# Kernel tuning notes

Measured on AMD Instinct MI355X. Metric: run time of the kernel, lower is better.

The kernel has to match this reference:

```python
import jax, jax.numpy as jnp
import numpy as np

STRIDE = 16
SCALES = (8, 16, 32)
RATIOS = (0.5, 1.0, 2.0)
PRE_NMS_TOPN = 6000
POST_NMS_TOPN = 300
NMS_THRESH = 0.7
MIN_SIZE = 16.0


def _mkanchors(ws, hs, xc, yc):
    ws = ws[:, None]; hs = hs[:, None]
    return np.hstack([xc - 0.5 * (ws - 1), yc - 0.5 * (hs - 1),
                      xc + 0.5 * (ws - 1), yc + 0.5 * (hs - 1)])


def _base_anchors():
    base = np.array([0.0, 0.0, STRIDE - 1.0, STRIDE - 1.0])
    w = base[2] - base[0] + 1; h = base[3] - base[1] + 1
    xc = base[0] + 0.5 * (w - 1); yc = base[1] + 0.5 * (h - 1)
    size = w * h
    ratios = np.array(RATIOS)
    ws = np.round(np.sqrt(size / ratios)); hs = np.round(ws * ratios)
    ra = _mkanchors(ws, hs, xc, yc)  # [3,4]
    out = []
    for a in ra:
        aw = a[2] - a[0] + 1; ah = a[3] - a[1] + 1
        axc = a[0] + 0.5 * (aw - 1); ayc = a[1] + 0.5 * (ah - 1)
        s = np.array(SCALES)
        out.append(_mkanchors(aw * s, ah * s, axc, ayc))
    return np.vstack(out).astype(np.float32)  # [9,4]


def _all_anchors(H, W):
    base = _base_anchors()  # [A,4]
    sx = np.arange(W) * STRIDE; sy = np.arange(H) * STRIDE
    gx, gy = np.meshgrid(sx, sy)  # [H,W]
    shifts = np.stack([gx.ravel(), gy.ravel(), gx.ravel(), gy.ravel()], axis=1)
    return (shifts[:, None, :].astype(np.float32) + base[None, :, :]).reshape(-1, 4)


def conv2d(x, w, b, pad):
    y = jax.lax.conv_general_dilated(x, w, (1, 1), [(pad, pad), (pad, pad)],
                                     dimension_numbers=('NCHW', 'OIHW', 'NCHW'))
    return y + b[None, :, None, None]


def rpn_forward(feature_map, im_info, conv_w, conv_b, cls_w, cls_b, bbox_w, bbox_b):
    x = jax.nn.relu(conv2d(feature_map, conv_w, conv_b, 1))
    cls_score = conv2d(x, cls_w, cls_b, 0)   # [1, 2A, H, W]
    bbox_pred = conv2d(x, bbox_w, bbox_b, 0)  # [1, 4A, H, W]
    b, c, H, W = cls_score.shape
    A = c // 2
    # softmax over (bg, fg) pairs: view(b,2,A,H,W), softmax dim=1
    prob = jax.nn.softmax(cls_score.reshape(b, 2, A, H, W), axis=1).reshape(b, c, H, W)
    scores = prob[0, A:].transpose(1, 2, 0).reshape(-1)       # fg scores [H*W*A]
    deltas = bbox_pred[0].transpose(1, 2, 0).reshape(-1, 4)   # [H*W*A, 4]
    anchors = jnp.asarray(_all_anchors(H, W))

    # bbox_transform_inv
    aw = anchors[:, 2] - anchors[:, 0] + 1.0
    ah = anchors[:, 3] - anchors[:, 1] + 1.0
    acx = anchors[:, 0] + 0.5 * aw
    acy = anchors[:, 1] + 0.5 * ah
    cx = deltas[:, 0] * aw + acx
    cy = deltas[:, 1] * ah + acy
    pw = jnp.exp(deltas[:, 2]) * aw
    ph = jnp.exp(deltas[:, 3]) * ah
    # clip to image
    x1 = jnp.clip(cx - 0.5 * pw, 0.0, im_info[1] - 1.0)
    y1 = jnp.clip(cy - 0.5 * ph, 0.0, im_info[0] - 1.0)
    x2 = jnp.clip(cx + 0.5 * pw, 0.0, im_info[1] - 1.0)
    y2 = jnp.clip(cy + 0.5 * ph, 0.0, im_info[0] - 1.0)
    boxes = jnp.stack([x1, y1, x2, y2], axis=1)

    # min-size filter (mask via -inf scores to keep shapes static)
    ms = MIN_SIZE * im_info[2]
    keep = ((x2 - x1 + 1.0) >= ms) & ((y2 - y1 + 1.0) >= ms)
    scores = jnp.where(keep, scores, -jnp.inf)

    # pre-NMS top-k (sorted descending)
    sc, idx = jax.lax.top_k(scores, PRE_NMS_TOPN)
    bx = boxes[idx]  # [P,4]
    areas = (bx[:, 2] - bx[:, 0] + 1.0) * (bx[:, 3] - bx[:, 1] + 1.0)

    def nms_step(supp, _):
        avail = jnp.where(supp, -jnp.inf, sc)
        i = jnp.argmax(avail)
        valid = avail[i] > -jnp.inf
        box = bx[i]
        xx1 = jnp.maximum(box[0], bx[:, 0]); yy1 = jnp.maximum(box[1], bx[:, 1])
        xx2 = jnp.minimum(box[2], bx[:, 2]); yy2 = jnp.minimum(box[3], bx[:, 3])
        inter = jnp.maximum(xx2 - xx1 + 1.0, 0.0) * jnp.maximum(yy2 - yy1 + 1.0, 0.0)
        iou = inter / (areas[i] + areas - inter)
        supp = supp | (iou > NMS_THRESH)  # suppresses i itself (iou==1)
        out_box = jnp.where(valid, box, jnp.zeros((4,), box.dtype))
        return supp, out_box

    supp0 = jnp.zeros((PRE_NMS_TOPN,), dtype=bool)
    _, kept = jax.lax.scan(nms_step, supp0, None, length=POST_NMS_TOPN)  # [300,4]
    rois = jnp.concatenate([jnp.zeros((POST_NMS_TOPN, 1), kept.dtype), kept], axis=1)
    return rois  # [300, 5] (batch_idx, x1, y1, x2, y2)


def setup_inputs() -> dict:
    key = jax.random.key(0)
    ks = jax.random.split(key, 7)
    C, A = 512, 9
    H, W = 64, 96  # feature map for a 1024x1536 image at stride 16
    std = 0.01  # weight_init gaussian std in the repo
    return {
        'feature_map': jax.random.normal(ks[0], (1, C, H, W), jnp.float32),
        'im_info': jnp.array([1024.0, 1536.0, 1.0], jnp.float32),
        'conv_w': std * jax.random.normal(ks[1], (C, C, 3, 3), jnp.float32),
        'conv_b': jnp.zeros((C,), jnp.float32),
        'cls_w': std * jax.random.normal(ks[2], (2 * A, C, 1, 1), jnp.float32),
        'cls_b': jnp.zeros((2 * A,), jnp.float32),
        'bbox_w': std * jax.random.normal(ks[3], (4 * A, C, 1, 1), jnp.float32),
        'bbox_b': jnp.zeros((4 * A,), jnp.float32),
    }


def reference(feature_map, im_info, conv_w, conv_b, cls_w, cls_b, bbox_w, bbox_b):
    return rpn_forward(feature_map, im_info, conv_w, conv_b, cls_w, cls_b, bbox_w, bbox_b)
```

## Files before the change

### kernel.cpp

```cpp
#include <hip/hip_runtime.h>
#include <stdint.h>

typedef unsigned int u32;
typedef unsigned long long u64;
typedef __attribute__((ext_vector_type(8))) short v8s;
typedef __attribute__((ext_vector_type(4))) float v4f;

#define HH 64
#define WW 96
#define HW 6144
#define CC 512
#define NANCH 55296
#define PRE 6000
#define POST 300
#define CAP 8192
#define PW 98
#define PH 66
#define ICPAD 40
#define NHB 384

__device__ __constant__ float c_aw[9] = {184.f,368.f,736.f,128.f,256.f,512.f,88.f,176.f,352.f};
__device__ __constant__ float c_ah[9] = {96.f,192.f,384.f,128.f,256.f,512.f,176.f,352.f,704.f};

__device__ __forceinline__ unsigned short bf16_rne(float x){
  u32 u = __float_as_uint(x);
  return (unsigned short)((u + 0x7FFFu + ((u >> 16) & 1u)) >> 16);
}
__device__ __forceinline__ u32 sortkey(float s){
  u32 u = __float_as_uint(s);
  return u ^ ((u & 0x80000000u) ? 0xFFFFFFFFu : 0x80000000u);
}

__global__ __launch_bounds__(256) void k_cvt(const float* __restrict__ X, const float* __restrict__ Wt,
                                             const float* __restrict__ cw, const float* __restrict__ bw,
                                             unsigned short* __restrict__ Xih, unsigned short* __restrict__ Xil,
                                             unsigned short* __restrict__ Wh2, unsigned short* __restrict__ Wl2,
                                             float* __restrict__ Whd, u32* __restrict__ zero_region){
  __shared__ float Ls[64][97];
  __shared__ float Ws[4608];
  const int b = blockIdx.x, tid = threadIdx.x;
  { int gid = b*256 + tid;
    if (gid < 163856) zero_region[gid] = 0u; }
  if (b < 528){
    const int rp  = b % 66;
    const int ic0 = (b / 66) * 64;
    const bool zrow = (rp == 0 || rp == PH-1);
    if (!zrow){
      int r = rp - 1;
      for (int i = tid; i < 6144; i += 256){
        int ii = i / 96, c = i - ii*96;
        Ls[ii][c] = X[(ic0+ii)*HW + r*WW + c];
      }
    }
    __syncthreads();
    for (int idx = tid; idx < 98*16; idx += 256){
      int cp = idx >> 4, g = idx & 15;
      int icl0 = g*4;
      u64 hv = 0, lv = 0;
      #pragma unroll
      for (int u = 0; u < 4; ++u){
        float x = 0.f;
        if (!zrow && cp >= 1 && cp <= 96) x = Ls[icl0+u][cp-1];
        unsigned short h = bf16_rne(x);
        float hf = __uint_as_float(((u32)h) << 16);
        unsigned short l = bf16_rne(x - hf);
        hv |= ((u64)h) << (16*u);
        lv |= ((u64)l) << (16*u);
      }
      long o = ((long)(rp*PW + cp) << 9) + ic0 + icl0;
      *reinterpret_cast<u64*>(Xih + o) = hv;
      *reinterpret_cast<u64*>(Xil + o) = lv;
    }
  } else if (b < 1040){
    const int oc = b - 528;
    for (int i = tid; i < 4608; i += 256) Ws[i] = Wt[oc*4608 + i];
    __syncthreads();
    for (int idx = tid; idx < 9*128; idx += 256){
      int tap = idx >> 7, g = idx & 127;
      int icb = g*4;
      u64 hv = 0, lv = 0;
      #pragma unroll
      for (int u = 0; u < 4; ++u){
        float x = Ws[(icb+u)*9 + tap];
        unsigned short h = bf16_rne(x);
        float hf = __uint_as_float(((u32)h) << 16);
        unsigned short l = bf16_rne(x - hf);
        hv |= ((u64)h) << (16*u);
        lv |= ((u64)l) << (16*u);
      }
      long o = ((long)(tap*512 + oc) << 9) + icb;
      *reinterpret_cast<u64*>(Wh2 + o) = hv;
      *reinterpret_cast<u64*>(Wl2 + o) = lv;
    }
  } else {
    int idx = (b - 1040)*256 + tid;
    int o  = idx >> 9;
    int gc = idx & 511;
    float v = 0.f;
    if (o < 18) v = cw[o*512 + gc];
    else if (o < 54) v = bw[(o-18)*512 + gc];
    Whd[gc*64 + o] = v;
  }
}

template<bool FIRST, bool LAST>
__global__ __launch_bounds__(256, 1) void k_conv3t(
    const unsigned short* __restrict__ Xih, const unsigned short* __restrict__ Xil,
    const unsigned short* __restrict__ Wh2, const unsigned short* __restrict__ Wl2,
    const float* __restrict__ Bc, float* __restrict__ Y)
{
  __shared__ __attribute__((aligned(16))) unsigned short Ah[6*98*ICPAD];
  __shared__ __attribute__((aligned(16))) unsigned short Al[6*98*ICPAD];
  __shared__ __attribute__((aligned(16))) unsigned short Bh[9*32*ICPAD];
  __shared__ __attribute__((aligned(16))) unsigned short Bl[9*32*ICPAD];
  const int tid  = threadIdx.x;
  const int w    = tid >> 6;
  const int lane = tid & 63;
  const int lm   = lane & 15;
  const int q    = lane >> 4;
  const int y0   = blockIdx.x * 4;
  const int oc0  = blockIdx.y * 32;
  const int yrow = y0 + w;

  v4f acc[6][2];
  if (FIRST){
    #pragma unroll
    for (int t = 0; t < 6; ++t)
      #pragma unroll
      for (int n = 0; n < 2; ++n)
        acc[t][n] = (v4f){0.f,0.f,0.f,0.f};
  } else {
    #pragma unroll
    for (int n = 0; n < 2; ++n){
      int oc = oc0 + n*16 + lm;
      #pragma unroll
      for (int t = 0; t < 6; ++t)
        acc[t][n] = *reinterpret_cast<const v4f*>(Y + (long)oc*HW + yrow*WW + 16*t + q*4);
    }
  }

  const int icg0 = FIRST ? 0 : 8;
  const int icgN = LAST ? 16 : 8;

  u64 ra[19][2], rb[9][2];
  auto loadSlab = [&](int icg){
    #pragma unroll
    for (int n = 0; n < 19; ++n){
      int it = tid + 256*n;
      if (it < 4704){
        int i4 = it & 7, rc = it >> 3;
        int c = rc % 98, r = rc / 98;
        long src = ((long)((y0 + r)*PW + c) << 9) + icg*32 + i4*4;
        ra[n][0] = *reinterpret_cast<const u64*>(Xih + src);
        ra[n][1] = *reinterpret_cast<const u64*>(Xil + src);
      }
    }
    #pragma unroll
    for (int n = 0; n < 9; ++n){
      int it = tid + 256*n;
      if (it < 2304){
        int i4 = it & 7, to = it >> 3;
        int oc = to & 31, tap = to >> 5;
        long src = ((long)(tap*512 + oc0 + oc) << 9) + icg*32 + i4*4;
        rb[n][0] = *reinterpret_cast<const u64*>(Wh2 + src);
        rb[n][1] = *reinterpret_cast<const u64*>(Wl2 + src);
      }
    }
  };
  auto storeSlab = [&](){
    #pragma unroll
    for (int n = 0; n < 19; ++n){
      int it = tid + 256*n;
      if (it < 4704){
        int i4 = it & 7, rc = it >> 3;
        int dst = rc*ICPAD + i4*4;
        *reinterpret_cast<u64*>(Ah + dst) = ra[n][0];
        *reinterpret_cast<u64*>(Al + dst) = ra[n][1];
      }
    }
    #pragma unroll
    for (int n = 0; n < 9; ++n){
      int it = tid + 256*n;
      if (it < 2304){
        int i4 = it & 7, to = it >> 3;
        int dst = to*ICPAD + i4*4;
        *reinterpret_cast<u64*>(Bh + dst) = rb[n][0];
        *reinterpret_cast<u64*>(Bl + dst) = rb[n][1];
      }
    }
  };

  loadSlab(icg0);
  for (int icg = icg0; icg < icgN; ++icg){
    __syncthreads();
    storeSlab();
    __syncthreads();
    if (icg + 1 < icgN) loadSlab(icg + 1);
    #pragma unroll
    for (int tap = 0; tap < 9; ++tap){
      const int dy = tap / 3, dx = tap - dy*3;
      v8s ah[6], al[6], bh[2], bl[2];
      #pragma unroll
      for (int t = 0; t < 6; ++t){
        int a = ((w + dy)*98 + 16*t + lm + dx)*ICPAD + q*8;
        ah[t] = *reinterpret_cast<const v8s*>(Ah + a);
        al[t] = *reinterpret_cast<const v8s*>(Al + a);
      }
      #pragma unroll
      for (int n = 0; n < 2; ++n){
        int a = (tap*32 + n*16 + lm)*ICPAD + q*8;
        bh[n] = *reinterpret_cast<const v8s*>(Bh + a);
        bl[n] = *reinterpret_cast<const v8s*>(Bl + a);
      }
      #pragma unroll
      for (int t = 0; t < 6; ++t)
        #pragma unroll
        for (int n = 0; n < 2; ++n){
          acc[t][n] = __builtin_amdgcn_mfma_f32_16x16x32_bf16(al[t], bl[n], acc[t][n], 0, 0, 0);
          acc[t][n] = __builtin_amdgcn_mfma_f32_16x16x32_bf16(al[t], bh[n], acc[t][n], 0, 0, 0);
          acc[t][n] = __builtin_amdgcn_mfma_f32_16x16x32_bf16(ah[t], bl[n], acc[t][n], 0, 0, 0);
          acc[t][n] = __builtin_amdgcn_mfma_f32_16x16x32_bf16(ah[t], bh[n], acc[t][n], 0, 0, 0);
        }
    }
  }

  #pragma unroll
  for (int n = 0; n < 2; ++n){
    int oc = oc0 + n*16 + lm;
    if (LAST){
      float b = Bc[oc];
      #pragma unroll
      for (int t = 0; t < 6; ++t){
        float4 v;
        v.x = fmaxf(acc[t][n].x + b, 0.f);
        v.y = fmaxf(acc[t][n].y + b, 0.f);
        v.z = fmaxf(acc[t][n].z + b, 0.f);
        v.w = fmaxf(acc[t][n].w + b, 0.f);
        *reinterpret_cast<float4*>(Y + (long)oc*HW + yrow*WW + 16*t + q*4) = v;
      }
    } else {
      #pragma unroll
      for (int t = 0; t < 6; ++t)
        *reinterpret_cast<v4f*>(Y + (long)oc*HW + yrow*WW + 16*t + q*4) = acc[t][n];
    }
  }
}

__global__ __launch_bounds__(256) void k_head(
    const float* __restrict__ Y, const float* __restrict__ Whd,
    const float* __restrict__ cb, const float* __restrict__ bb,
    const float* __restrict__ info,
    float* __restrict__ scores, float4* __restrict__ boxes, u32* __restrict__ hist8g)
{
  __shared__ float Ys[1024];
  __shared__ float Wsh[4096];
  __shared__ u32 lh[256];
  const int tid = threadIdx.x;
  const int p0  = blockIdx.x * 16;
  const int po  = tid & 15;
  const int oj  = tid >> 4;
  lh[tid] = 0u;
  float accM[4], accC[4];
  #pragma unroll
  for (int k = 0; k < 4; ++k){ accM[k] = 0.f; accC[k] = 0.f; }

  for (int c0 = 0; c0 < CC; c0 += 64){
    __syncthreads();
    for (int i = tid; i < 1024; i += 256){
      int c = i >> 4, p = i & 15;
      Ys[i] = Y[(c0 + c) * HW + p0 + p];
    }
    for (int i = tid; i < 4096; i += 256){
      int c = i >> 6, o = i & 63;
      Wsh[c*64 + (o & 15)*4 + (o >> 4)] = Whd[(c0 + c)*64 + o];
    }
    __syncthreads();
    #pragma unroll 4
    for (int c = 0; c < 64; ++c){
      float xa = Ys[c*16 + po];
      float4 wv = *reinterpret_cast<const float4*>(Wsh + c*64 + oj*4);
      accC[0] = __fmaf_rn(xa, wv.x, accC[0]);
      accC[1] = __fmaf_rn(xa, wv.y, accC[1]);
      accC[2] = __fmaf_rn(xa, wv.z, accC[2]);
      accC[3] = __fmaf_rn(xa, wv.w, accC[3]);
    }
    #pragma unroll
    for (int k = 0; k < 4; ++k){ accM[k] += accC[k]; accC[k] = 0.f; }
  }
  __syncthreads();
  #pragma unroll
  for (int k = 0; k < 4; ++k){
    int o = oj + 16*k;
    float bias = (o < 18) ? cb[o] : ((o < 54) ? bb[o - 18] : 0.f);
    Ys[po*64 + o] = accM[k] + bias;
  }
  __syncthreads();
  float imH = info[0], imW = info[1], imS = info[2];
  for (int it = tid; it < 144; it += 256){
    int pl = it / 9;
    int a  = it - pl*9;
    const float* L = Ys + pl*64;
    float l0 = L[a], l1 = L[9 + a];
    float mx = fmaxf(l0, l1);
    float e0 = expf(l0 - mx), e1 = expf(l1 - mx);
    float sc = e1 / (e0 + e1);
    float d0 = L[18 + a*4 + 0], d1 = L[18 + a*4 + 1];
    float d2 = L[18 + a*4 + 2], d3 = L[18 + a*4 + 3];
    int pos = p0 + pl;
    int yy = pos / 96;
    int xx = pos - yy * 96;
    float aw = c_aw[a], ah = c_ah[a];
    float acx = (float)(xx * 16 + 8);
    float acy = (float)(yy * 16 + 8);
    float cx = __fadd_rn(__fmul_rn(d0, aw), acx);
    float cy = __fadd_rn(__fmul_rn(d1, ah), acy);
    float pw = __fmul_rn(expf(d2), aw);
    float ph = __fmul_rn(expf(d3), ah);
    float hx = __fmul_rn(0.5f, pw);
    float hy = __fmul_rn(0.5f, ph);
    float x1 = fminf(fmaxf(__fadd_rn(cx, -hx), 0.f), imW - 1.f);
    float y1 = fminf(fmaxf(__fadd_rn(cy, -hy), 0.f), imH - 1.f);
    float x2 = fminf(fmaxf(__fadd_rn(cx,  hx), 0.f), imW - 1.f);
    float y2 = fminf(fmaxf(__fadd_rn(cy,  hy), 0.f), imH - 1.f);
    float ms = 16.f * imS;
    bool keep = ((x2 - x1 + 1.f) >= ms) && ((y2 - y1 + 1.f) >= ms);
    int g = pos * 9 + a;
    float val = keep ? sc : -__builtin_inff();
    scores[g] = val;
    boxes[g]  = make_float4(x1, y1, x2, y2);
    atomicAdd(&lh[sortkey(val) >> 24], 1u);
  }
  __syncthreads();
  hist8g[blockIdx.x*256 + tid] = lh[tid];
}

__global__ __launch_bounds__(1024) void k_sel(const u32* __restrict__ hist8g, u32* __restrict__ hist2,
                                              const float* __restrict__ scores,
                                              u32* __restrict__ ctr, u64* __restrict__ keys){
  __shared__ u32 cs[1024];
  __shared__ u32 bs[64];
  __shared__ u32 h8[256];
  __shared__ u32 lh2[256];
  __shared__ int selg;
  __shared__ u32 afterv, T16s, aboves, K32s, B8s, above8s;
  const int t = threadIdx.x;
  const int b0 = t * 64;

  { int g = t >> 8, bin = t & 255;
    u32 s = 0;
    for (int b = g; b < NHB; b += 4) s += hist8g[b*256 + bin];
    cs[t] = s; }
  __syncthreads();
  if (t < 256){
    h8[t] = cs[t] + cs[256 + t] + cs[512 + t] + cs[768 + t];
    lh2[t] = 0u;
  }
  __syncthreads();
  if (t == 0){
    u32 acc = 0;
    for (int bin = 255; bin >= 0; --bin){
      acc += h8[bin];
      if (acc >= 6000u){ B8s = (u32)bin; above8s = acc - h8[bin]; break; }
    }
  }
  __syncthreads();

  { u32 b8 = B8s;
    const float4* s4 = reinterpret_cast<const float4*>(scores);
    for (int i = t; i < NANCH/4; i += 1024){
      float4 v = s4[i];
      u32 k0 = sortkey(v.x), k1 = sortkey(v.y), k2 = sortkey(v.z), k3 = sortkey(v.w);
      if ((k0 >> 24) == b8) atomicAdd(&lh2[(k0 >> 16) & 0xFFu], 1u);
      if ((k1 >> 24) == b8) atomicAdd(&lh2[(k1 >> 16) & 0xFFu], 1u);
      if ((k2 >> 24) == b8) atomicAdd(&lh2[(k2 >> 16) & 0xFFu], 1u);
      if ((k3 >> 24) == b8) atomicAdd(&lh2[(k3 >> 16) & 0xFFu], 1u);
    } }
  __syncthreads();
  if (t == 0){
    u32 acc = above8s;
    for (int bin = 255; bin >= 0; --bin){
      acc += lh2[bin];
      if (acc >= 6000u){ T16s = (B8s << 8) | (u32)bin; aboves = acc - lh2[bin]; break; }
    }
  }
  __syncthreads();

  { u32 pfx = T16s;
    const float4* s4 = reinterpret_cast<const float4*>(scores);
    for (int i = t; i < NANCH/4; i += 1024){
      float4 v = s4[i];
      u32 k0 = sortkey(v.x), k1 = sortkey(v.y), k2 = sortkey(v.z), k3 = sortkey(v.w);
      if ((k0 >> 16) == pfx) atomicAdd(&hist2[k0 & 0xFFFFu], 1u);
      if ((k1 >> 16) == pfx) atomicAdd(&hist2[k1 & 0xFFFFu], 1u);
      if ((k2 >> 16) == pfx) atomicAdd(&hist2[k2 & 0xFFFFu], 1u);
      if ((k3 >> 16) == pfx) atomicAdd(&hist2[k3 & 0xFFFFu], 1u);
    } }
  __threadfence();
  __syncthreads();

  if (t == 0) selg = -1;
  __syncthreads();
  const u32 target = 6000u - aboves;
  { u32 s = 0;
    for (int i = 0; i < 64; ++i) s += hist2[b0 + i];
    cs[t] = s; }
  __syncthreads();
  for (int off = 1; off < 1024; off <<= 1){
    u32 v = cs[t];
    u32 ad = (t + off < 1024) ? cs[t + off] : 0u;
    __syncthreads();
    cs[t] = v + ad;
    __syncthreads();
  }
  { u32 here  = cs[t];
    u32 after = (t < 1023) ? cs[t + 1] : 0u;
    if (here >= target && after < target){ selg = t; afterv = after; } }
  __syncthreads();
  { int g = selg;
    if (g >= 0 && t < 64) bs[t] = hist2[g*64 + t];
    __syncthreads();
    if (t == 0){
      if (g < 0) K32s = (T16s << 16);
      else {
        u32 acc = afterv;
        for (int b = 63; b >= 0; --b){
          u32 h = bs[b];
          acc += h;
          if (acc >= target){ K32s = (T16s << 16) | (u32)(g*64 + b); break; }
        }
      }
      ctr[4] = 6000u;
    } }
  __syncthreads();

  { u32 K = K32s;
    const int lane = t & 63;
    const float4* s4 = reinterpret_cast<const float4*>(scores);
    for (int i = t; i < NANCH/4; i += 1024){
      float4 v = s4[i];
      u32 kk[4] = {sortkey(v.x), sortkey(v.y), sortkey(v.z), sortkey(v.w)};
      u64 m[4];
      #pragma unroll
      for (int u = 0; u < 4; ++u) m[u] = __ballot(kk[u] >= K);
      u32 tot = (u32)(__popcll(m[0]) + __popcll(m[1]) + __popcll(m[2]) + __popcll(m[3]));
      if (tot){
        u32 base = 0;
        if (lane == 0) base = atomicAdd(&ctr[0], tot);
        base = (u32)__shfl((int)base, 0, 64);
        u64 below = ((u64)1 << lane) - 1;
        u32 off = 0;
        #pragma unroll
        for (int u = 0; u < 4; ++u){
          if (kk[u] >= K){
            u32 pos = base + off + (u32)__popcll(m[u] & below);
            if (pos < CAP) keys[pos] = ((u64)kk[u] << 32) | (u64)(u32)(~(u32)(i*4 + u));
          }
          off += (u32)__popcll(m[u]);
        }
      }
    } }
}

__global__ __launch_bounds__(512) void k_rank(const u64* __restrict__ keys, u32* __restrict__ ctr,
                                              const float4* __restrict__ boxes,
                                              float4* __restrict__ topB, float* __restrict__ topA){
  __shared__ u64 ks[CAP];
  __shared__ u32 part[8][64];
  const int t  = threadIdx.x;
  const int s  = t >> 6;
  const int k  = t & 63;
  const int gi = blockIdx.x * 64 + k;
  u32 count = ctr[0]; if (count > CAP) count = CAP;
  u64 my = (gi < (int)count) ? keys[gi] : 0ull;
  for (int j = t; j < CAP; j += 512)
    ks[j] = (j < (int)count) ? keys[j] : 0ull;
  __syncthreads();
  int rank = 0;
  { const ulonglong2* kp = reinterpret_cast<const ulonglong2*>(ks + s*1024);
    #pragma unroll 8
    for (int j = 0; j < 512; ++j){
      ulonglong2 kv = kp[j];
      rank += (kv.x > my) + (kv.y > my);
    } }
  part[s][k] = (u32)rank;
  __syncthreads();
  if (t < 64){
    int r = 0;
    #pragma unroll
    for (int ss = 0; ss < 8; ++ss) r += part[ss][k];
    bool sel = (gi < (int)count && r < PRE);
    int myv = 0x7FFFFFFF;
    if (sel && !((my >> 32) & 0x80000000ull)) myv = r;
    #pragma unroll
    for (int off = 32; off; off >>= 1){
      int o = __shfl_down(myv, off, 64);
      myv = (o < myv) ? o : myv;
    }
    if (k == 0 && myv != 0x7FFFFFFF) atomicMin((int*)(ctr + 4), myv);
    if (sel){
      u32 idx = ~(u32)my;
      float4 bv = make_float4(0.f,0.f,0.f,0.f);
      float area = 1.f;
      if (idx < NANCH){
        bv = boxes[idx];
        area = (bv.z - bv.x + 1.f) * (bv.w - bv.y + 1.f);
      }
      topB[r] = bv;
      topA[r] = area;
    }
  }
}

__global__ __launch_bounds__(256) void k_nms3(const float4* __restrict__ topB,
                                              const u32* __restrict__ ctr, float* __restrict__ out){
  __shared__ float4 kb[POST];
  __shared__ float4 bx2[64];
  __shared__ u64    am[4];
  __shared__ int    nkS;
  const int tid  = threadIdx.x;
  const int wv   = tid >> 6;
  const int lane = tid & 63;
  int validN = (int)ctr[0];
  int finN   = (int)ctr[4];
  if (finN < validN) validN = finN;
  if (validN > PRE)  validN = PRE;
  if (tid == 0) nkS = 0;
  __syncthreads();

  float4 bnx = make_float4(0.f,0.f,0.f,0.f);
  if (lane < validN) bnx = topB[lane];

  for (int base = 0; base < validN; base += 64){
    int nk = nkS;
    if (nk >= POST) break;
    int c = base + lane;
    bool alive = (c < validN);
    float4 b = bnx;
    float ar = alive ? (b.z - b.x + 1.f) * (b.w - b.y + 1.f) : 1.f;
    if (wv == 0) bx2[lane] = b;
    { int cn = base + 64 + lane;
      if (cn < validN) bnx = topB[cn]; }
    int j = wv;
    for (; j + 28 < nk; j += 32){
      float4 kx[8];
      #pragma unroll
      for (int u = 0; u < 8; ++u) kx[u] = kb[j + 4*u];
      #pragma unroll
      for (int u = 0; u < 8; ++u){
        float kar = (kx[u].z - kx[u].x + 1.f) * (kx[u].w - kx[u].y + 1.f);
        float xx1 = fmaxf(kx[u].x, b.x);
        float yy1 = fmaxf(kx[u].y, b.y);
        float xx2 = fminf(kx[u].z, b.z);
        float yy2 = fminf(kx[u].w, b.w);
        float iw = fmaxf(xx2 - xx1 + 1.f, 0.f);
        float ih = fmaxf(yy2 - yy1 + 1.f, 0.f);
        float inter = iw * ih;
        float iou = inter / (kar + ar - inter);
        if (iou > 0.7f) alive = false;
      }
    }
    for (; j < nk; j += 4){
      float4 kbx = kb[j];
      float kar = (kbx.z - kbx.x + 1.f) * (kbx.w - kbx.y + 1.f);
      float xx1 = fmaxf(kbx.x, b.x);
      float yy1 = fmaxf(kbx.y, b.y);
      float xx2 = fminf(kbx.z, b.z);
      float yy2 = fminf(kbx.w, b.w);
      float iw = fmaxf(xx2 - xx1 + 1.f, 0.f);
      float ih = fmaxf(yy2 - yy1 + 1.f, 0.f);
      float inter = iw * ih;
      float iou = inter / (kar + ar - inter);
      if (iou > 0.7f) alive = false;
    }
    { u64 bal = __ballot(alive);
      if (lane == 0) am[wv] = bal; }
    __syncthreads();
    if (wv == 0){
      u64 comb = am[0] & am[1] & am[2] & am[3];
      alive = ((comb >> lane) & 1ull) != 0ull;
      int nkl = nk;
      while (nkl < POST){
        u64 bal = __ballot(alive);
        if (!bal) break;
        int L = (int)__ffsll((unsigned long long)bal) - 1;
        float4 pb = bx2[L];
        float pa = (pb.z - pb.x + 1.f) * (pb.w - pb.y + 1.f);
        if (lane == 0) kb[nkl] = pb;
        nkl++;
        if (lane == L) alive = false;
        if (alive){
          float xx1 = fmaxf(pb.x, b.x);
          float yy1 = fmaxf(pb.y, b.y);
          float xx2 = fminf(pb.z, b.z);
          float yy2 = fminf(pb.w, b.w);
          float iw = fmaxf(xx2 - xx1 + 1.f, 0.f);
          float ih = fmaxf(yy2 - yy1 + 1.f, 0.f);
          float inter = iw * ih;
          float iou = inter / (pa + ar - inter);
          if (iou > 0.7f) alive = false;
        }
      }
      if (lane == 0) nkS = nkl;
    }
    __syncthreads();
  }
  int nk = nkS;
  for (int q = tid; q < 1500; q += 256){
    int r = q / 5, c = q - r*5;
    float v = 0.f;
    if (r < nk && c > 0){
      float4 bx = kb[r];
      v = (c == 1) ? bx.x : (c == 2) ? bx.y : (c == 3) ? bx.z : bx.w;
    }
    out[q] = v;
  }
}

extern "C" void kernel_launch(void* const* d_in, const int* in_sizes, int n_in,
                              void* d_out, int out_size, void* d_ws, size_t ws_size,
                              hipStream_t stream)
{
  const float* fm   = (const float*)d_in[0];
  const float* info = (const float*)d_in[1];
  const float* cw3  = (const float*)d_in[2];
  const float* cb3  = (const float*)d_in[3];
  const float* clw  = (const float*)d_in[4];
  const float* clb  = (const float*)d_in[5];
  const float* bbw  = (const float*)d_in[6];
  const float* bbb  = (const float*)d_in[7];
  float* out = (float*)d_out;

  char* base = (char*)d_ws;
  u32*   hist8g = (u32*)  (base + 0);
  u32*   hist2  = (u32*)  (base + 393216);
  u32*   ctr    = (u32*)  (base + 655360);
  float* Y      = (float*)(base + 655424);
  float* scores = (float*)(base + 13238336);
  float4* boxes = (float4*)(base + 13459520);
  u64*   keys   = (u64*)  (base + 14344256);
  float4* topB  = (float4*)(base + 14409792);
  float* topA   = (float*)(base + 14505792);
  unsigned short* Xih = (unsigned short*)(base + 14529792);
  unsigned short* Xil = (unsigned short*)(base + 21153024);
  unsigned short* Wh2 = (unsigned short*)(base + 27776256);
  unsigned short* Wl2 = (unsigned short*)(base + 32494848);
  float* Whd = (float*)(base + 37213440);

  k_cvt   <<<1168, 256, 0, stream>>>(fm, cw3, clw, bbw, Xih, Xil, Wh2, Wl2, Whd, (u32*)base);
  k_conv3t<true,false>  <<<dim3(16, 16), 256, 0, stream>>>(Xih, Xil, Wh2, Wl2, cb3, Y);
  k_conv3t<false,true>  <<<dim3(16, 16), 256, 0, stream>>>(Xih, Xil, Wh2, Wl2, cb3, Y);
  k_head  <<<384, 256, 0, stream>>>(Y, Whd, clb, bbb, info, scores, boxes, hist8g);
  k_sel   <<<1,  1024, 0, stream>>>(hist8g, hist2, scores, ctr, keys);
  k_rank  <<<128, 512, 0, stream>>>(keys, ctr, boxes, topB, topA);
  k_nms3  <<<1,   256, 0, stream>>>(topB, ctr, out);
}
```

Baseline: 407.2 us.

## Replace serial greedy NMS with parallel IoU bitmask plus single-wave scan

Splits NMS into two kernels. A grid-wide kernel computes the full upper-triangular 6000x6000 IoU suppression bitmask into workspace, reusing the Xih buffer region. A single 64-lane wave then scans the mask greedily until 300 boxes are kept. This moves the O(N*keep) IoU work from one block to the whole GPU. In exchange it computes all pairs, even though the old loop could stop early, and adds a serial chain of dependent global row loads per kept box.

```diff
diff --git a/kernel.cpp b/kernel.cpp
--- a/kernel.cpp
+++ b/kernel.cpp
@@ -18,6 +18,7 @@
 #define PH 66
 #define ICPAD 40
 #define NHB 384
+#define NW 94
 
 __device__ __constant__ float c_aw[9] = {184.f,368.f,736.f,128.f,256.f,512.f,88.f,176.f,352.f};
 __device__ __constant__ float c_ah[9] = {96.f,192.f,384.f,128.f,256.f,512.f,176.f,352.f,704.f};
@@ -511,105 +512,97 @@
   }
 }
 
-__global__ __launch_bounds__(256) void k_nms3(const float4* __restrict__ topB,
-                                              const u32* __restrict__ ctr, float* __restrict__ out){
-  __shared__ float4 kb[POST];
-  __shared__ float4 bx2[64];
-  __shared__ u64    am[4];
-  __shared__ int    nkS;
-  const int tid  = threadIdx.x;
-  const int wv   = tid >> 6;
-  const int lane = tid & 63;
+__global__ __launch_bounds__(256) void k_mask(const float4* __restrict__ topB,
+                                              u64* __restrict__ mask){
+  int id = blockIdx.x * 256 + threadIdx.x;
+  if (id >= NW * PRE) return;
+  int w = id / PRE;
+  int i = id - w * PRE;
+  if (w * 64 + 63 <= i){
+    mask[(long)i * NW + w] = 0ull;
+    return;
+  }
+  float4 bi = topB[i];
+  float ai = (bi.z - bi.x + 1.f) * (bi.w - bi.y + 1.f);
+  u64 bits = 0;
+  #pragma unroll 8
+  for (int jj = 0; jj < 64; ++jj){
+    int j = w * 64 + jj;
+    if (j < PRE){
+      float4 bj = topB[j];
+      float aj = (bj.z - bj.x + 1.f) * (bj.w - bj.y + 1.f);
+      float xx1 = fmaxf(bi.x, bj.x);
+      float yy1 = fmaxf(bi.y, bj.y);
+      float xx2 = fminf(bi.z, bj.z);
+      float yy2 = fminf(bi.w, bj.w);
+      float iw = fmaxf(xx2 - xx1 + 1.f, 0.f);
+      float ih = fmaxf(yy2 - yy1 + 1.f, 0.f);
+      float inter = iw * ih;
+      float iou = inter / (ai + aj - inter);
+      if (iou > 0.7f) bits |= (1ull << jj);
+    }
+  }
+  mask[(long)i * NW + w] = bits;
+}
+
+__global__ __launch_bounds__(64) void k_nms4(const float4* __restrict__ topB,
+                                             const u32* __restrict__ ctr,
+                                             const u64* __restrict__ mask,
+                                             float* __restrict__ out){
+  __shared__ int kidx[POST];
+  const int lane = threadIdx.x;
   int validN = (int)ctr[0];
   int finN   = (int)ctr[4];
   if (finN < validN) validN = finN;
   if (validN > PRE)  validN = PRE;
-  if (tid == 0) nkS = 0;
-  __syncthreads();
-
-  float4 bnx = make_float4(0.f,0.f,0.f,0.f);
-  if (lane < validN) bnx = topB[lane];
-
-  for (int base = 0; base < validN; base += 64){
-    int nk = nkS;
-    if (nk >= POST) break;
-    int c = base + lane;
-    bool alive = (c < validN);
-    float4 b = bnx;
-    float ar = alive ? (b.z - b.x + 1.f) * (b.w - b.y + 1.f) : 1.f;
-    if (wv == 0) bx2[lane] = b;
-    { int cn = base + 64 + lane;
-      if (cn < validN) bnx = topB[cn]; }
-    int j = wv;
-    for (; j + 28 < nk; j += 32){
-      float4 kx[8];
-      #pragma unroll
-      for (int u = 0; u < 8; ++u) kx[u] = kb[j + 4*u];
-      #pragma unroll
-      for (int u = 0; u < 8; ++u){
-        float kar = (kx[u].z - kx[u].x + 1.f) * (kx[u].w - kx[u].y + 1.f);
-        float xx1 = fmaxf(kx[u].x, b.x);
-        float yy1 = fmaxf(kx[u].y, b.y);
-        float xx2 = fminf(kx[u].z, b.z);
-        float yy2 = fminf(kx[u].w, b.w);
-        float iw = fmaxf(xx2 - xx1 + 1.f, 0.f);
-        float ih = fmaxf(yy2 - yy1 + 1.f, 0.f);
-        float inter = iw * ih;
-        float iou = inter / (kar + ar - inter);
-        if (iou > 0.7f) alive = false;
-      }
-    }
-    for (; j < nk; j += 4){
-      float4 kbx = kb[j];
-      float kar = (kbx.z - kbx.x + 1.f) * (kbx.w - kbx.y + 1.f);
-      float xx1 = fmaxf(kbx.x, b.x);
-      float yy1 = fmaxf(kbx.y, b.y);
-      float xx2 = fminf(kbx.z, b.z);
-      float yy2 = fminf(kbx.w, b.w);
-      float iw = fmaxf(xx2 - xx1 + 1.f, 0.f);
-      float ih = fmaxf(yy2 - yy1 + 1.f, 0.f);
-      float inter = iw * ih;
-      float iou = inter / (kar + ar - inter);
-      if (iou > 0.7f) alive = false;
-    }
-    { u64 bal = __ballot(alive);
-      if (lane == 0) am[wv] = bal; }
-    __syncthreads();
-    if (wv == 0){
-      u64 comb = am[0] & am[1] & am[2] & am[3];
-      alive = ((comb >> lane) & 1ull) != 0ull;
-      int nkl = nk;
-      while (nkl < POST){
-        u64 bal = __ballot(alive);
-        if (!bal) break;
-        int L = (int)__ffsll((unsigned long long)bal) - 1;
-        float4 pb = bx2[L];
-        float pa = (pb.z - pb.x + 1.f) * (pb.w - pb.y + 1.f);
-        if (lane == 0) kb[nkl] = pb;
-        nkl++;
-        if (lane == L) alive = false;
-        if (alive){
-          float xx1 = fmaxf(pb.x, b.x);
-          float yy1 = fmaxf(pb.y, b.y);
-          float xx2 = fminf(pb.z, b.z);
-          float yy2 = fminf(pb.w, b.w);
-          float iw = fmaxf(xx2 - xx1 + 1.f, 0.f);
-          float ih = fmaxf(yy2 - yy1 + 1.f, 0.f);
-          float inter = iw * ih;
-          float iou = inter / (pa + ar - inter);
-          if (iou > 0.7f) alive = false;
+
+  auto initw = [&](int w)->u64 {
+    int base = w * 64;
+    if (base + 64 <= validN) return 0ull;
+    if (base >= validN) return ~0ull;
+    return (~0ull) << (validN - base);
+  };
+  u64 sa = initw(lane);
+  u64 sb = (lane < 30) ? initw(64 + lane) : ~0ull;
+
+  int nk = 0, cur = 0;
+  while (nk < POST){
+    int i = -1;
+    { const int cw = cur >> 6, cb = cur & 63;
+      u64 ma = ~sa;
+      if (lane < cw) ma = 0ull;
+      else if (lane == cw) ma &= (~0ull) << cb;
+      u64 bal = __ballot(ma != 0ull);
+      if (bal){
+        int wl = (int)__ffsll((unsigned long long)bal) - 1;
+        u64 mw = (u64)__shfl((long long)ma, wl, 64);
+        i = wl * 64 + (int)__ffsll((unsigned long long)mw) - 1;
+      } else {
+        u64 mb = (lane < 30) ? ~sb : 0ull;
+        int w2 = 64 + lane;
+        if (w2 < cw) mb = 0ull;
+        else if (w2 == cw) mb &= (~0ull) << cb;
+        u64 bal2 = __ballot(mb != 0ull);
+        if (bal2){
+          int wl = (int)__ffsll((unsigned long long)bal2) - 1;
+          u64 mw = (u64)__shfl((long long)mb, wl, 64);
+          i = (64 + wl) * 64 + (int)__ffsll((unsigned long long)mw) - 1;
         }
       }
-      if (lane == 0) nkS = nkl;
-    }
-    __syncthreads();
-  }
-  int nk = nkS;
-  for (int q = tid; q < 1500; q += 256){
+    }
+    if (i < 0) break;
+    if (lane == 0) kidx[nk] = i;
+    nk++; cur = i + 1;
+    const u64* row = mask + (long)i * NW;
+    sa |= row[lane];
+    if (lane < 30) sb |= row[64 + lane];
+  }
+  __syncthreads();
+  for (int q = lane; q < 1500; q += 64){
     int r = q / 5, c = q - r*5;
     float v = 0.f;
     if (r < nk && c > 0){
-      float4 bx = kb[r];
+      float4 bx = topB[kidx[r]];
       v = (c == 1) ? bx.x : (c == 2) ? bx.y : (c == 3) ? bx.z : bx.w;
     }
     out[q] = v;
@@ -645,6 +638,7 @@
   unsigned short* Wh2 = (unsigned short*)(base + 27776256);
   unsigned short* Wl2 = (unsigned short*)(base + 32494848);
   float* Whd = (float*)(base + 37213440);
+  u64* mask = (u64*)(base + 14529792);
 
   k_cvt   <<<1168, 256, 0, stream>>>(fm, cw3, clw, bbw, Xih, Xil, Wh2, Wl2, Whd, (u32*)base);
   k_conv3t<true,false>  <<<dim3(16, 16), 256, 0, stream>>>(Xih, Xil, Wh2, Wl2, cb3, Y);
@@ -652,5 +646,6 @@
   k_head  <<<384, 256, 0, stream>>>(Y, Whd, clb, bbb, info, scores, boxes, hist8g);
   k_sel   <<<1,  1024, 0, stream>>>(hist8g, hist2, scores, ctr, keys);
   k_rank  <<<128, 512, 0, stream>>>(keys, ctr, boxes, topB, topA);
-  k_nms3  <<<1,   256, 0, stream>>>(topB, ctr, out);
-}
+  k_mask  <<<(NW*PRE + 255)/256, 256, 0, stream>>>(topB, mask);
+  k_nms4  <<<1, 64, 0, stream>>>(topB, ctr, mask, out);
+}
```

Result: slower. 500.1 us (+22.8%).
